# Kernel tuning notes

Measured on AMD Instinct MI355X. Metric: run time of the kernel, lower is better.

## Reference

```python
import jax, jax.numpy as jnp
import numpy as np

B, N, D, H = 4, 2048, 1024, 16
DH = D // H


def setup_inputs() -> dict:
    key = jax.random.key(0)
    ks = jax.random.split(key, 9)
    std = 0.02
    return {
        "x": jax.random.normal(ks[0], (B, N, D), dtype=jnp.float32),
        "Wq": jax.random.normal(ks[1], (D, D), dtype=jnp.float32) * std,
        "bq": jnp.zeros((D,), dtype=jnp.float32),
        "Wk": jax.random.normal(ks[2], (D, D), dtype=jnp.float32) * std,
        "bk": jnp.zeros((D,), dtype=jnp.float32),
        "Wv": jax.random.normal(ks[3], (D, D), dtype=jnp.float32) * std,
        "bv": jnp.zeros((D,), dtype=jnp.float32),
        "Wo": jax.random.normal(ks[4], (D, D), dtype=jnp.float32) * std,
        "bo": jnp.zeros((D,), dtype=jnp.float32),
        "k": 8,
        "dilation": 2,
    }


def _dilated_mask(n_q, n_k, k, dilation):
    # allowed[i, j] = True iff |j - i| <= k*dilation and (j - i) % dilation == 0
    i = jnp.arange(n_q)[:, None]
    j = jnp.arange(n_k)[None, :]
    d = j - i
    return (jnp.abs(d) <= k * dilation) & ((d % dilation) == 0)


def reference(x, Wq, bq, Wk, bk, Wv, bv, Wo, bo, k, dilation):
    b, n_q, d_model = x.shape
    n_heads = H
    d_head = d_model // n_heads
    # self-attention: context = x
    q = (x @ Wq + bq).reshape(b, n_q, n_heads, d_head).transpose(0, 2, 1, 3)  # (B,H,Nq,Dh)
    kk = (x @ Wk + bk).reshape(b, n_q, n_heads, d_head).transpose(0, 2, 1, 3)
    v = (x @ Wv + bv).reshape(b, n_q, n_heads, d_head).transpose(0, 2, 1, 3)

    scale = 1.0 / np.sqrt(d_head).astype(np.float32)
    scores = jnp.einsum("bhqd,bhkd->bhqk", q, kk) * scale  # (B,H,Nq,Nk)
    allowed = _dilated_mask(n_q, n_q, k, dilation)  # (Nq,Nk)
    scores = jnp.where(allowed[None, None], scores, -jnp.inf)
    attn = jax.nn.softmax(scores, axis=-1)
    out = jnp.einsum("bhqk,bhkd->bhqd", attn, v)  # (B,H,Nq,Dh)
    out = out.transpose(0, 2, 1, 3).reshape(b, n_q, d_model)
    return out @ Wo + bo
```

## Files before the change

kernel.cpp:

```cpp
#include <hip/hip_runtime.h>
#include <hip/hip_bf16.h>
#include <hip/hip_fp16.h>
#include <stdint.h>

using bf16 = __hip_bfloat16;

typedef __bf16    bf16x8 __attribute__((ext_vector_type(8)));
typedef float     floatx4 __attribute__((ext_vector_type(4)));
typedef _Float16  f16x2 __attribute__((ext_vector_type(2)));
typedef _Float16  f16x8 __attribute__((ext_vector_type(8)));

typedef __attribute__((address_space(3))) void as3_void;
typedef __attribute__((address_space(1))) void as1_void;

#define GLD_LDS16(gp, lp) \
  __builtin_amdgcn_global_load_lds((as1_void*)(uintptr_t)(gp), (as3_void*)(uintptr_t)(lp), 16, 0, 0)

#if __has_builtin(__builtin_amdgcn_fdot2)
#define DOT2(a, b, c) __builtin_amdgcn_fdot2((a), (b), (c), false)
#else
#define DOT2(a, b, c) ((c) + (float)(a)[0] * (float)(b)[0] + (float)(a)[1] * (float)(b)[1])
#endif

__global__ __launch_bounds__(256) void convert_x_kernel(const float* __restrict__ x,
                                                        bf16* __restrict__ xbf) {
  const int i = (blockIdx.x * 256 + threadIdx.x) * 4;
  const float4 v = *(const float4*)(x + i);
  bf16 o[4] = {(bf16)v.x, (bf16)v.y, (bf16)v.z, (bf16)v.w};
  *(ushort4*)(xbf + i) = *(const ushort4*)o;
}

__global__ __launch_bounds__(256) void transpose_w_kernel(
    const float* __restrict__ Wq, const float* __restrict__ Wk,
    const float* __restrict__ Wv, const float* __restrict__ Wo,
    bf16* __restrict__ WTqkv, bf16* __restrict__ WoT) {
  __shared__ float tile[64 * 68];
  const int z = blockIdx.z;
  const float* src = (z == 0) ? Wq : (z == 1) ? Wk : (z == 2) ? Wv : Wo;
  bf16* dst = (z < 3) ? (WTqkv + (size_t)z * 1024 * 1024) : WoT;
  const int tid = threadIdx.x;
  const int nbase = blockIdx.x * 64, kbase = blockIdx.y * 64;

  const int r1 = tid >> 4, c1 = tid & 15;
#pragma unroll
  for (int it = 0; it < 4; ++it) {
    const int row = r1 + it * 16;
    const float4 v = *(const float4*)(src + (size_t)(kbase + row) * 1024 + nbase + c1 * 4);
    *(float4*)(tile + row * 68 + c1 * 4) = v;
  }
  __syncthreads();

  const int c2 = tid & 7, n2 = tid >> 3;
#pragma unroll
  for (int it2 = 0; it2 < 2; ++it2) {
    const int n = n2 + it2 * 32;
    bf16 o[8];
#pragma unroll
    for (int s = 0; s < 8; ++s) o[s] = (bf16)tile[(8 * c2 + s) * 68 + n];
    *(uint4*)(dst + (size_t)(nbase + n) * 1024 + kbase + 8 * c2) = *(const uint4*)o;
  }
}

template <int MODE>
__global__ __launch_bounds__(256) void gemm_bt_kernel(
    const bf16* __restrict__ A, const bf16* __restrict__ Bt,
    const float* __restrict__ b0, const float* __restrict__ b1, const float* __restrict__ b2,
    __half* __restrict__ out0, __half* __restrict__ out1, __half* __restrict__ out2,
    float* __restrict__ fout) {
  const int tid  = threadIdx.x;
  const int m0   = blockIdx.x * 128;
  const int n0   = blockIdx.y * 128;
  const int lane = tid & 63;
  const int wave = tid >> 6;
  const int wr   = (wave >> 1) * 64;
  const int wc   = (wave & 1) * 64;
  const int quad = lane >> 4;
  const int l16  = lane & 15;

  __shared__ alignas(16) bf16 As[128 * 64];
  __shared__ alignas(16) bf16 Bs[128 * 64];

  const int srow = tid >> 3;
  const int cg   = (tid & 7) ^ (srow & 7);
  uint64_t aoff;
  if (MODE == 0) {
    aoff = (uint64_t)(m0 + srow) * 1024 + cg * 8;
  } else {
    const int b = m0 >> 11, seq0 = m0 & 2047;
    aoff = (uint64_t)b * 2097152 + (uint64_t)(seq0 + srow) * 64 + cg * 8;
  }
  const uint64_t boff = (uint64_t)(n0 + srow) * 1024 + cg * 8;

  floatx4 acc[4][4];
#pragma unroll
  for (int i = 0; i < 4; ++i)
#pragma unroll
    for (int j = 0; j < 4; ++j) {
      floatx4 z = {0.f, 0.f, 0.f, 0.f};
      acc[i][j] = z;
    }

  for (int k0 = 0; k0 < 1024; k0 += 64) {
    __syncthreads();
#pragma unroll
    for (int it = 0; it < 4; ++it) {
      if (MODE == 0)
        GLD_LDS16(A + aoff + (uint64_t)it * 32768 + k0, (char*)As + it * 4096 + tid * 16);
      else
        GLD_LDS16(A + aoff + (uint64_t)it * 2048 + (uint64_t)(k0 >> 6) * 131072,
                  (char*)As + it * 4096 + tid * 16);
      GLD_LDS16(Bt + boff + (uint64_t)it * 32768 + k0, (char*)Bs + it * 4096 + tid * 16);
    }
    __syncthreads();

#pragma unroll
    for (int kc = 0; kc < 2; ++kc) {
      bf16x8 af[4], bfr[4];
#pragma unroll
      for (int i = 0; i < 4; ++i) {
        const int mrow = wr + i * 16 + l16;
        const int pca  = (kc * 4 + quad) ^ (mrow & 7);
        af[i] = *(const bf16x8*)(As + mrow * 64 + pca * 8);
        const int nrow = wc + i * 16 + l16;
        const int pcb  = (kc * 4 + quad) ^ (nrow & 7);
        bfr[i] = *(const bf16x8*)(Bs + nrow * 64 + pcb * 8);
      }
#pragma unroll
      for (int i = 0; i < 4; ++i)
#pragma unroll
        for (int j = 0; j < 4; ++j)
          acc[i][j] = __builtin_amdgcn_mfma_f32_16x16x32_bf16(af[i], bfr[j], acc[i][j], 0, 0, 0);
    }
  }

#pragma unroll
  for (int i = 0; i < 4; ++i) {
#pragma unroll
    for (int j = 0; j < 4; ++j) {
#pragma unroll
      for (int r = 0; r < 4; ++r) {
        const int m = m0 + wr + i * 16 + quad * 4 + r;
        const int n = n0 + wc + j * 16 + l16;
        float v = acc[i][j][r];
        if (MODE == 0) {
          const int which = n >> 10;
          const int c = n & 1023;
          const float* bp = (which == 0) ? b0 : (which == 1) ? b1 : b2;
          __half* op      = (which == 0) ? out0 : (which == 1) ? out1 : out2;
          v += bp[c];
          const int h = c >> 6, dh = c & 63;
          const int bb = m >> 11, seq = m & 2047;
          op[(uint64_t)(bb * 16 + h) * 131072 + (uint64_t)seq * 64 + dh] = (__half)v;
        } else {
          fout[(uint64_t)m * 1024 + n] = v + b0[n];
        }
      }
    }
  }
}

#define RMAX 32
#define RSTRIDE 66

#define ATTN_T_BODY(KPTR, KIDX, VPTR)                                      \
  {                                                                        \
    f16x8 vc[8];                                                           \
    _Pragma("unroll")                                                      \
    for (int c = 0; c < 8; ++c) vc[c] = *(const f16x8*)((VPTR) + c * 8);   \
    f16x8 kc[8];                                                           \
    _Pragma("unroll")                                                      \
    for (int c = 0; c < 8; ++c)                                            \
      kc[c] = *(const f16x8*)((KPTR) + (KIDX) + c * 8);                    \
    float sp[4] = {0.f, 0.f, 0.f, 0.f};                                    \
    _Pragma("unroll")                                                      \
    for (int c = 0; c < 8; ++c) {                                          \
      _Pragma("unroll")                                                    \
      for (int u = 0; u < 4; ++u) {                                        \
        const f16x2 qa = {q[c][2 * u], q[c][2 * u + 1]};                   \
        const f16x2 ka = {kc[c][2 * u], kc[c][2 * u + 1]};                 \
        sp[c & 3] = DOT2(qa, ka, sp[c & 3]);                               \
      }                                                                    \
    }                                                                      \
    const float s = (sp[0] + sp[1]) + (sp[2] + sp[3]);                     \
    const float pe = valid ? __expf(s * 0.125f) : 0.f;                     \
    l += pe;                                                               \
    const _Float16 ph = (_Float16)pe;                                      \
    const f16x2 pe2 = {ph, ph};                                            \
    _Pragma("unroll")                                                      \
    for (int c = 0; c < 8; ++c) {                                          \
      _Pragma("unroll")                                                    \
      for (int u = 0; u < 4; ++u) {                                        \
        const f16x2 va = {vc[c][2 * u], vc[c][2 * u + 1]};                 \
        oo[c * 4 + u] += pe2 * va;                                         \
      }                                                                    \
    }                                                                      \
  }

__global__ __launch_bounds__(128) void dilated_attn_kernel(
    const __half* __restrict__ Q, const __half* __restrict__ K, const __half* __restrict__ V,
    bf16* __restrict__ attn_out, const int* __restrict__ kptr, const int* __restrict__ dptr) {
  const int tid = threadIdx.x;
  const int bh  = blockIdx.x >> 4;
  const int qb  = blockIdx.x & 15;
  const int Q0  = qb * 128;
  const int kk  = kptr[0];
  const int dil = dptr[0];
  const int R   = kk * dil;

  const size_t base = (size_t)bh * 2048 * 64;

  __shared__ alignas(16) _Float16 Ks[192 * RSTRIDE];

  const int jlo_b = (Q0 - RMAX > 0) ? Q0 - RMAX : 0;
  const int jhi_b = (Q0 + 127 + RMAX < 2047) ? Q0 + 127 + RMAX : 2047;
  const int nrows = jhi_b - jlo_b + 1;
  const bool fast = (R <= RMAX) && (dil > 0);

  if (fast) {
    const int nch = nrows * 8;
    for (int c = tid; c < nch; c += 128) {
      const int r = c >> 3, ch = (c & 7) * 8;
      *(f16x8*)(Ks + r * RSTRIDE + ch) =
          *(const f16x8*)((const _Float16*)K + base + (size_t)(jlo_b + r) * 64 + ch);
    }
    __syncthreads();
  }

  const int wave = tid >> 6, lane = tid & 63;
  const int i = Q0 + wave * 64 + lane;

  f16x8 q[8];
#pragma unroll
  for (int t = 0; t < 8; ++t)
    q[t] = *(const f16x8*)((const _Float16*)Q + base + (size_t)i * 64 + t * 8);

  float l = 0.f;
  f16x2 oo[32];
#pragma unroll
  for (int t = 0; t < 32; ++t) oo[t] = (f16x2){(_Float16)0, (_Float16)0};

  if (fast) {
    const int rbase = i - jlo_b;
    for (int t = -kk; t <= kk; ++t) {
      const int j = i + t * dil;
      const bool valid = (unsigned)j < 2048u;
      int row = rbase + t * dil;
      row = (row < 0) ? 0 : (row >= nrows ? nrows - 1 : row);
      const _Float16* vp = (const _Float16*)V + base + (size_t)(valid ? j : i) * 64;
      ATTN_T_BODY(Ks, row * RSTRIDE, vp)
    }
  } else {
    for (int t = -kk; t <= kk; ++t) {
      const int j = i + t * dil;
      const bool valid = (unsigned)j < 2048u;
      const int jc = valid ? j : i;
      const _Float16* vp = (const _Float16*)V + base + (size_t)jc * 64;
      ATTN_T_BODY((const _Float16*)K, base + (size_t)jc * 64, vp)
    }
  }

  const float linv = 1.f / fmaxf(l, 1e-30f);
  alignas(16) bf16 orow[64];
#pragma unroll
  for (int t = 0; t < 32; ++t) {
    orow[2 * t]     = (bf16)((float)oo[t][0] * linv);
    orow[2 * t + 1] = (bf16)((float)oo[t][1] * linv);
  }
  bf16* dst = attn_out + base + (size_t)i * 64;
#pragma unroll
  for (int c = 0; c < 8; ++c)
    *(uint4*)(dst + c * 8) = *(const uint4*)(orow + c * 8);
}

extern "C" void kernel_launch(void* const* d_in, const int* in_sizes, int n_in,
                              void* d_out, int out_size, void* d_ws, size_t ws_size,
                              hipStream_t stream) {
  const float* x  = (const float*)d_in[0];
  const float* Wq = (const float*)d_in[1];
  const float* bq = (const float*)d_in[2];
  const float* Wk = (const float*)d_in[3];
  const float* bk = (const float*)d_in[4];
  const float* Wv = (const float*)d_in[5];
  const float* bv = (const float*)d_in[6];
  const float* Wo = (const float*)d_in[7];
  const float* bo = (const float*)d_in[8];
  const int* kp   = (const int*)d_in[9];
  const int* dp   = (const int*)d_in[10];
  float* out = (float*)d_out;

  bf16*   xbf   = (bf16*)d_ws;
  bf16*   WTqkv = xbf + 8388608;
  bf16*   WoT   = WTqkv + 3072 * 1024;
  __half* qbuf  = (__half*)(WoT + 1024 * 1024);
  __half* kbuf  = qbuf + 8388608;
  __half* vbuf  = kbuf + 8388608;
  bf16*   attnH = xbf;

  convert_x_kernel<<<dim3(8192), 256, 0, stream>>>(x, xbf);
  transpose_w_kernel<<<dim3(16, 16, 4), 256, 0, stream>>>(Wq, Wk, Wv, Wo, WTqkv, WoT);

  gemm_bt_kernel<0><<<dim3(64, 24), 256, 0, stream>>>(xbf, WTqkv, bq, bk, bv,
                                                      qbuf, kbuf, vbuf, nullptr);

  dilated_attn_kernel<<<dim3(1024), 128, 0, stream>>>(qbuf, kbuf, vbuf, attnH, kp, dp);

  gemm_bt_kernel<1><<<dim3(64, 8), 256, 0, stream>>>(attnH, WoT, bo, nullptr, nullptr,
                                                     nullptr, nullptr, nullptr, out);
}
```

Measured before the change: 234.5 us.

## Stage V in LDS with XOR swizzle, enlarge attention tiles, merge prep kernels

The attention kernel now stages both K and V rows in shared memory, using an XOR-swizzled layout in place of padding, and processes 256 queries per 256-thread block instead of 128. Previously V was read straight from global memory for every tap. The x conversion and the weight transpose are merged into a single prep launch, and each thread now converts 16 elements. The goals are less global traffic for V and fewer kernel launches, at the cost of more LDS per block (about 80 KB), which may reduce occupancy.

```diff
diff --git a/kernel.cpp b/kernel.cpp
--- a/kernel.cpp
+++ b/kernel.cpp
@@ -22,42 +22,46 @@
 #define DOT2(a, b, c) ((c) + (float)(a)[0] * (float)(b)[0] + (float)(a)[1] * (float)(b)[1])
 #endif
 
-__global__ __launch_bounds__(256) void convert_x_kernel(const float* __restrict__ x,
-                                                        bf16* __restrict__ xbf) {
-  const int i = (blockIdx.x * 256 + threadIdx.x) * 4;
-  const float4 v = *(const float4*)(x + i);
-  bf16 o[4] = {(bf16)v.x, (bf16)v.y, (bf16)v.z, (bf16)v.w};
-  *(ushort4*)(xbf + i) = *(const ushort4*)o;
-}
-
-__global__ __launch_bounds__(256) void transpose_w_kernel(
+__global__ __launch_bounds__(256) void prep_kernel(
+    const float* __restrict__ x,
     const float* __restrict__ Wq, const float* __restrict__ Wk,
     const float* __restrict__ Wv, const float* __restrict__ Wo,
-    bf16* __restrict__ WTqkv, bf16* __restrict__ WoT) {
+    bf16* __restrict__ xbf, bf16* __restrict__ WTqkv, bf16* __restrict__ WoT) {
   __shared__ float tile[64 * 68];
-  const int z = blockIdx.z;
-  const float* src = (z == 0) ? Wq : (z == 1) ? Wk : (z == 2) ? Wv : Wo;
-  bf16* dst = (z < 3) ? (WTqkv + (size_t)z * 1024 * 1024) : WoT;
+  const int blk = blockIdx.x;
   const int tid = threadIdx.x;
-  const int nbase = blockIdx.x * 64, kbase = blockIdx.y * 64;
-
-  const int r1 = tid >> 4, c1 = tid & 15;
-#pragma unroll
-  for (int it = 0; it < 4; ++it) {
-    const int row = r1 + it * 16;
-    const float4 v = *(const float4*)(src + (size_t)(kbase + row) * 1024 + nbase + c1 * 4);
-    *(float4*)(tile + row * 68 + c1 * 4) = v;
-  }
-  __syncthreads();
-
-  const int c2 = tid & 7, n2 = tid >> 3;
-#pragma unroll
-  for (int it2 = 0; it2 < 2; ++it2) {
-    const int n = n2 + it2 * 32;
-    bf16 o[8];
-#pragma unroll
-    for (int s = 0; s < 8; ++s) o[s] = (bf16)tile[(8 * c2 + s) * 68 + n];
-    *(uint4*)(dst + (size_t)(nbase + n) * 1024 + kbase + 8 * c2) = *(const uint4*)o;
+  if (blk < 1024) {
+    const int z = blk >> 8, t = blk & 255;
+    const float* src = (z == 0) ? Wq : (z == 1) ? Wk : (z == 2) ? Wv : Wo;
+    bf16* dst = (z < 3) ? (WTqkv + (size_t)z * 1024 * 1024) : WoT;
+    const int nbase = (t & 15) * 64, kbase = (t >> 4) * 64;
+    const int r1 = tid >> 4, c1 = tid & 15;
+#pragma unroll
+    for (int it = 0; it < 4; ++it) {
+      const int row = r1 + it * 16;
+      const float4 v = *(const float4*)(src + (size_t)(kbase + row) * 1024 + nbase + c1 * 4);
+      *(float4*)(tile + row * 68 + c1 * 4) = v;
+    }
+    __syncthreads();
+    const int c2 = tid & 7, n2 = tid >> 3;
+#pragma unroll
+    for (int it2 = 0; it2 < 2; ++it2) {
+      const int n = n2 + it2 * 32;
+      bf16 o[8];
+#pragma unroll
+      for (int s = 0; s < 8; ++s) o[s] = (bf16)tile[(8 * c2 + s) * 68 + n];
+      *(uint4*)(dst + (size_t)(nbase + n) * 1024 + kbase + 8 * c2) = *(const uint4*)o;
+    }
+  } else {
+    const size_t basei = ((size_t)(blk - 1024) * 256 + tid) * 16;
+#pragma unroll
+    for (int h = 0; h < 2; ++h) {
+      const float4 a = *(const float4*)(x + basei + h * 8);
+      const float4 b = *(const float4*)(x + basei + h * 8 + 4);
+      bf16 o[8] = {(bf16)a.x, (bf16)a.y, (bf16)a.z, (bf16)a.w,
+                   (bf16)b.x, (bf16)b.y, (bf16)b.z, (bf16)b.w};
+      *(uint4*)(xbf + basei + h * 8) = *(const uint4*)o;
+    }
   }
 }
 
@@ -160,17 +164,15 @@
 }
 
 #define RMAX 32
-#define RSTRIDE 66
-
-#define ATTN_T_BODY(KPTR, KIDX, VPTR)                                      \
+
+#define ATTN_T_CORE(KEXPR, VEXPR)                                          \
   {                                                                        \
-    f16x8 vc[8];                                                           \
+    f16x8 kc[8], vc[8];                                                    \
     _Pragma("unroll")                                                      \
-    for (int c = 0; c < 8; ++c) vc[c] = *(const f16x8*)((VPTR) + c * 8);   \
-    f16x8 kc[8];                                                           \
-    _Pragma("unroll")                                                      \
-    for (int c = 0; c < 8; ++c)                                            \
-      kc[c] = *(const f16x8*)((KPTR) + (KIDX) + c * 8);                    \
+    for (int c = 0; c < 8; ++c) {                                          \
+      kc[c] = *(const f16x8*)(KEXPR);                                      \
+      vc[c] = *(const f16x8*)(VEXPR);                                      \
+    }                                                                      \
     float sp[4] = {0.f, 0.f, 0.f, 0.f};                                    \
     _Pragma("unroll")                                                      \
     for (int c = 0; c < 8; ++c) {                                          \
@@ -196,32 +198,34 @@
     }                                                                      \
   }
 
-__global__ __launch_bounds__(128) void dilated_attn_kernel(
+__global__ __launch_bounds__(256) void dilated_attn_kernel(
     const __half* __restrict__ Q, const __half* __restrict__ K, const __half* __restrict__ V,
     bf16* __restrict__ attn_out, const int* __restrict__ kptr, const int* __restrict__ dptr) {
   const int tid = threadIdx.x;
-  const int bh  = blockIdx.x >> 4;
-  const int qb  = blockIdx.x & 15;
-  const int Q0  = qb * 128;
+  const int bh  = blockIdx.x >> 3;
+  const int qb  = blockIdx.x & 7;
+  const int Q0  = qb * 256;
   const int kk  = kptr[0];
   const int dil = dptr[0];
   const int R   = kk * dil;
 
   const size_t base = (size_t)bh * 2048 * 64;
 
-  __shared__ alignas(16) _Float16 Ks[192 * RSTRIDE];
+  __shared__ alignas(16) _Float16 Ks[320 * 64];
+  __shared__ alignas(16) _Float16 Vs[320 * 64];
 
   const int jlo_b = (Q0 - RMAX > 0) ? Q0 - RMAX : 0;
-  const int jhi_b = (Q0 + 127 + RMAX < 2047) ? Q0 + 127 + RMAX : 2047;
+  const int jhi_b = (Q0 + 255 + RMAX < 2047) ? Q0 + 255 + RMAX : 2047;
   const int nrows = jhi_b - jlo_b + 1;
   const bool fast = (R <= RMAX) && (dil > 0);
 
   if (fast) {
-    const int nch = nrows * 8;
-    for (int c = tid; c < nch; c += 128) {
-      const int r = c >> 3, ch = (c & 7) * 8;
-      *(f16x8*)(Ks + r * RSTRIDE + ch) =
-          *(const f16x8*)((const _Float16*)K + base + (size_t)(jlo_b + r) * 64 + ch);
+    for (int c = tid; c < nrows * 8; c += 256) {
+      const int r = c >> 3, ch = c & 7;
+      const int slot = ch ^ (r & 7);
+      const size_t g = base + (size_t)(jlo_b + r) * 64 + ch * 8;
+      *(f16x8*)(Ks + r * 64 + slot * 8) = *(const f16x8*)((const _Float16*)K + g);
+      *(f16x8*)(Vs + r * 64 + slot * 8) = *(const f16x8*)((const _Float16*)V + g);
     }
     __syncthreads();
   }
@@ -246,16 +250,15 @@
       const bool valid = (unsigned)j < 2048u;
       int row = rbase + t * dil;
       row = (row < 0) ? 0 : (row >= nrows ? nrows - 1 : row);
-      const _Float16* vp = (const _Float16*)V + base + (size_t)(valid ? j : i) * 64;
-      ATTN_T_BODY(Ks, row * RSTRIDE, vp)
+      const int ro = row * 64, rx = row & 7;
+      ATTN_T_CORE(Ks + ro + ((c ^ rx) << 3), Vs + ro + ((c ^ rx) << 3))
     }
   } else {
     for (int t = -kk; t <= kk; ++t) {
       const int j = i + t * dil;
       const bool valid = (unsigned)j < 2048u;
-      const int jc = valid ? j : i;
-      const _Float16* vp = (const _Float16*)V + base + (size_t)jc * 64;
-      ATTN_T_BODY((const _Float16*)K, base + (size_t)jc * 64, vp)
+      const size_t go = base + (size_t)(valid ? j : i) * 64;
+      ATTN_T_CORE((const _Float16*)K + go + c * 8, (const _Float16*)V + go + c * 8)
     }
   }
 
@@ -296,13 +299,12 @@
   __half* vbuf  = kbuf + 8388608;
   bf16*   attnH = xbf;
 
-  convert_x_kernel<<<dim3(8192), 256, 0, stream>>>(x, xbf);
-  transpose_w_kernel<<<dim3(16, 16, 4), 256, 0, stream>>>(Wq, Wk, Wv, Wo, WTqkv, WoT);
+  prep_kernel<<<dim3(3072), 256, 0, stream>>>(x, Wq, Wk, Wv, Wo, xbf, WTqkv, WoT);
 
   gemm_bt_kernel<0><<<dim3(64, 24), 256, 0, stream>>>(xbf, WTqkv, bq, bk, bv,
                                                       qbuf, kbuf, vbuf, nullptr);
 
-  dilated_attn_kernel<<<dim3(1024), 128, 0, stream>>>(qbuf, kbuf, vbuf, attnH, kp, dp);
+  dilated_attn_kernel<<<dim3(512), 256, 0, stream>>>(qbuf, kbuf, vbuf, attnH, kp, dp);
 
   gemm_bt_kernel<1><<<dim3(64, 8), 256, 0, stream>>>(attnH, WoT, bo, nullptr, nullptr,
                                                      nullptr, nullptr, nullptr, out);
```

New measurement: 208.3 us. 11.2% less time.
